# Kernel optimization log

Hardware: AMD Instinct MI355X
Metric: run time of the kernel (lower is better)

## Reference

```python
import jax, jax.numpy as jnp
import numpy as np

B, K, S = 4096, 32, 6          # batch, n_neighbors, n_shifts
QD, H, NH = 512, 384, 6        # query_dim, hidden_dim, n_heads
HD = H // NH                   # head_dim
NR = 20                        # n_residue_types (table has NR+1 rows)
NBR_IN = S + S + 16 + 1 + 1    # neighbor_proj input dim = 30

def gelu(x):
    return jax.nn.gelu(x, approximate=False)

def setup_inputs():
    key = jax.random.key(0)
    ks = iter(jax.random.split(key, 64))
    def nrm(shape, scale=0.05):
        return jax.random.normal(next(ks), shape, dtype=jnp.float32) * scale
    inp = {}
    inp['query_encoding'] = jax.random.normal(next(ks), (B, QD), dtype=jnp.float32)
    inp['query_residue_code'] = jax.random.randint(next(ks), (B,), 0, NR + 1).astype(jnp.int32)
    inp['query_observed_shifts'] = jax.random.normal(next(ks), (B, S), dtype=jnp.float32)
    inp['query_shift_masks'] = (jax.random.uniform(next(ks), (B, S)) < 0.8).astype(jnp.float32)
    inp['retrieved_shifts'] = jax.random.normal(next(ks), (B, K, S), dtype=jnp.float32)
    inp['retrieved_shift_masks'] = jax.random.uniform(next(ks), (B, K, S)) < 0.8
    inp['retrieved_residue_codes'] = jax.random.randint(next(ks), (B, K), 0, NR + 1).astype(jnp.int32)
    inp['retrieved_distances'] = jax.random.uniform(next(ks), (B, K), dtype=jnp.float32)
    inp['retrieved_valid'] = jax.random.uniform(next(ks), (B, K)) < 0.9
    # parameters (buffers + weights). rc_table kept finite (no NaN rows sampled).
    inp['rc_table'] = nrm((NR + 1, S), 1.0)
    inp['W_qp'] = nrm((QD, H)); inp['b_qp'] = jnp.zeros((H,))
    inp['E_res'] = nrm((NR + 1, 16))
    inp['W_np'] = nrm((NBR_IN, H)); inp['b_np'] = jnp.zeros((H,))
    inp['W_aq'] = nrm((H, H)); inp['b_aq'] = jnp.zeros((H,))
    inp['W_ak'] = nrm((H, H)); inp['b_ak'] = jnp.zeros((H,))
    inp['W_av'] = nrm((H, H)); inp['b_av'] = jnp.zeros((H,))
    inp['W_ss1'] = nrm((2 * S, H // 2)); inp['b_ss1'] = jnp.zeros((H // 2,))
    inp['W_ss2'] = nrm((H // 2, NH)); inp['b_ss2'] = jnp.zeros((NH,))
    inp['W_cp1'] = nrm((H, H)); inp['b_cp1'] = jnp.zeros((H,))
    inp['W_cp2'] = nrm((H, H)); inp['b_cp2'] = jnp.zeros((H,))
    inp['W_sw1'] = nrm((H, H)); inp['b_sw1'] = jnp.zeros((H,))
    inp['W_sw2'] = nrm((H, S)); inp['b_sw2'] = jnp.zeros((S,))
    inp['E_trust'] = nrm((NR + 1, 32))
    inp['W_tq'] = nrm((QD, H)); inp['b_tq'] = jnp.zeros((H,))
    inp['W_tc'] = nrm((H + 32 + 4, H)); inp['b_tc'] = jnp.zeros((H,))
    inp['W_tp1'] = nrm((H + 4, H // 2)); inp['b_tp1'] = jnp.zeros((H // 2,))
    inp['W_tp2'] = nrm((H // 2, 1)); inp['b_tp2'] = jnp.zeros((1,))
    inp['shift_scale'] = jnp.ones((S,)); inp['fallback_shift'] = jnp.zeros((S,))
    inp['fallback_context'] = jnp.zeros((H,))
    return inp

def _forward(p):
    eps = 1e-8
    qcode = p['query_residue_code']; rcodes = p['retrieved_residue_codes']
    smask = p['retrieved_shift_masks']; valid = p['retrieved_valid']
    dist = p['retrieved_distances']; rc = p['rc_table']
    # --- RC correction: corrected = RC[query] + (shift - RC[retrieved]) ---
    qidx = jnp.clip(qcode, 0, rc.shape[0] - 1)
    ridx = jnp.clip(rcodes, 0, rc.shape[0] - 1)
    rc_q = rc[qidx][:, None, :]            # (B,1,S)
    rc_r = rc[ridx]                         # (B,K,S)
    corrected = rc_q + (p['retrieved_shifts'] - rc_r)
    rc_valid = (~jnp.isnan(rc_q)) & (~jnp.isnan(rc_r))
    corrected = jnp.where(rc_valid, corrected, p['retrieved_shifts'])
    shifts = jnp.where(smask, corrected, p['retrieved_shifts'])  # (B,K,S)
    any_valid = valid.any(axis=1)                                # (B,)
    same_type = (rcodes == qcode[:, None]).astype(jnp.float32)   # (B,K)
    # --- projections ---
    q = gelu(p['query_encoding'] @ p['W_qp'] + p['b_qp'])        # (B,H)
    res_emb = p['E_res'][rcodes]                                 # (B,K,16)
    nbr = jnp.concatenate([shifts, smask.astype(jnp.float32), res_emb,
                           dist[..., None], same_type[..., None]], axis=-1)
    kv = gelu(nbr @ p['W_np'] + p['b_np'])                       # (B,K,H)
    # --- multi-head cross attention (single query token) ---
    Qh = (q @ p['W_aq'] + p['b_aq']).reshape(B, NH, HD)
    Kh = (kv @ p['W_ak'] + p['b_ak']).reshape(B, K, NH, HD)
    Vh = (kv @ p['W_av'] + p['b_av']).reshape(B, K, NH, HD)
    scores = jnp.einsum('bhd,bkhd->bhk', Qh, Kh) * (HD ** -0.5)  # (B,NH,K)
    sdiff = jnp.concatenate([
        (p['query_observed_shifts'][:, None, :] - shifts) * p['query_shift_masks'][:, None, :],
        jnp.broadcast_to(p['query_shift_masks'][:, None, :], (B, K, S))], axis=-1)
    bias = gelu(sdiff @ p['W_ss1'] + p['b_ss1']) @ p['W_ss2'] + p['b_ss2']  # (B,K,NH)
    scores = scores + jnp.transpose(bias, (0, 2, 1))
    # if nothing valid, unmask slot 0 (matches torch all_masked fixup)
    valid_eff = valid | ((~any_valid)[:, None] & (jnp.arange(K) == 0)[None, :])
    scores = jnp.where(valid_eff[:, None, :], scores, -10000.0)
    w = jax.nn.softmax(scores, axis=-1)
    attn_out = jnp.einsum('bhk,bkhd->bhd', w, Vh).reshape(B, H)
    ctx = gelu(attn_out @ p['W_cp1'] + p['b_cp1']) @ p['W_cp2'] + p['b_cp2']
    ctx = jnp.where(any_valid[:, None], ctx, p['fallback_context'][None, :])
    # --- shift transfer ---
    swb = gelu(attn_out @ p['W_sw1'] + p['b_sw1']) @ p['W_sw2'] + p['b_sw2']  # (B,S)
    weights = dist[..., None] + same_type[..., None] * 0.5 + swb[:, None, :] * 0.1  # (B,K,S)
    valid_mask = valid[..., None] & smask
    weights = jnp.where(valid_mask, weights, -10000.0)
    weights = jax.nn.softmax(weights, axis=1)
    transferred = jnp.sum(weights * shifts, axis=1) * p['shift_scale']
    transferred = jnp.where(any_valid[:, None], transferred, p['fallback_shift'][None, :])
    # --- trust statistics (no grad in original) ---
    vm = valid_mask.astype(jnp.float32)
    cnt = vm.sum(axis=1)                                         # (B,S)
    cov = cnt / (K + eps)
    mean = (shifts * vm).sum(axis=1) / (cnt + eps)
    var = (((shifts - mean[:, None, :]) ** 2) * vm).sum(axis=1) / (cnt + eps)
    var_n = jnp.clip(jnp.log1p(var), 0.0, 5.0) / 5.0
    mdist = (dist[..., None] * vm).sum(axis=1) / (cnt + eps)
    stp = (same_type[..., None] * vm).sum(axis=1) / (cnt + eps)
    per_stats = jax.lax.stop_gradient(jnp.stack([cov, var_n, mdist, stp], axis=-1))  # (B,S,4)
    vf = valid.astype(jnp.float32)
    n_valid = vf.sum(axis=1, keepdims=True) / K
    n_same = (same_type * vf).sum(axis=1, keepdims=True) / K
    dmask = jnp.where(valid, dist, 0.0)
    gmean = dmask.sum(axis=1, keepdims=True) / (vf.sum(axis=1, keepdims=True) + eps)
    gmax = dmask.max(axis=1, keepdims=True)
    gstats = jax.lax.stop_gradient(jnp.concatenate([gmean, gmax, n_valid, n_same], axis=-1))  # (B,4)
    # --- trust head ---
    qre = p['E_trust'][qcode]                                    # (B,32)
    tq = gelu(p['query_encoding'] @ p['W_tq'] + p['b_tq'])
    tc = gelu(jnp.concatenate([tq, qre, gstats], axis=-1) @ p['W_tc'] + p['b_tc'])  # (B,H)
    tin = jnp.concatenate([jnp.broadcast_to(tc[:, None, :], (B, S, H)), per_stats], axis=-1)
    trust = jax.nn.sigmoid(gelu(tin @ p['W_tp1'] + p['b_tp1']) @ p['W_tp2'] + p['b_tp2'])[..., 0]
    return ctx, transferred, trust

def reference(query_encoding, query_residue_code, query_observed_shifts, query_shift_masks,
              retrieved_shifts, retrieved_shift_masks, retrieved_residue_codes,
              retrieved_distances, retrieved_valid, rc_table,
              W_qp, b_qp, E_res, W_np, b_np, W_aq, b_aq, W_ak, b_ak, W_av, b_av,
              W_ss1, b_ss1, W_ss2, b_ss2, W_cp1, b_cp1, W_cp2, b_cp2,
              W_sw1, b_sw1, W_sw2, b_sw2, E_trust, W_tq, b_tq, W_tc, b_tc,
              W_tp1, b_tp1, W_tp2, b_tp2, shift_scale, fallback_shift, fallback_context):
    return _forward(dict(locals()))
```

## Files before the change

### kernel.cpp

```cpp
#include <hip/hip_runtime.h>

typedef unsigned short u16;
typedef unsigned int u32;
typedef __attribute__((ext_vector_type(8))) short bf16x8;
typedef __attribute__((ext_vector_type(4))) float f32x4;

__device__ __forceinline__ float fs(float f) {
    return (f == f && fabsf(f) < 1e30f) ? f : 0.f;
}
__device__ __forceinline__ float fin(float v) {
    return (v == v && fabsf(v) < 1e30f) ? v : 555.0f;
}
__device__ __forceinline__ u16 f2b(float f) {
    union { float f; unsigned int i; } w; w.f = f;
    unsigned int r = w.i + 0x7FFFu + ((w.i >> 16) & 1u);
    return (u16)(r >> 16);
}
__device__ __forceinline__ float b2f(u16 b) {
    union { unsigned int i; float f; } w; w.i = ((unsigned int)b) << 16;
    return w.f;
}
__device__ __forceinline__ float gelu_f(float x) {
    return 0.5f * x * (1.0f + erff(x * 0.70710678118654752440f));
}

__global__ void fill_kernel(float* __restrict__ out, int n, float val) {
    int i = blockIdx.x * 256 + threadIdx.x;
    if (i < n) out[i] = val;
}

struct CvtSrcs { const float* p[13]; };

__global__ void k_cvt_all(CvtSrcs sp, u16* __restrict__ w) {
    int id = blockIdx.x * 256 + threadIdx.x;
    if (id >= 3634304) return;
    if (id < 2097152) { w[id] = f2b(fs(sp.p[0][id])); return; }
    if (id >= 2637824 && id < 2785280) { w[id] = f2b(fs(sp.p[4][id - 2637824])); return; }
    const float* src; int local, K, N, Kp;
    if (id < 2293760)      { src = sp.p[1];  local = id - 2097152; K = 512; N = 384; Kp = 512; }
    else if (id < 2490368) { src = sp.p[2];  local = id - 2293760; K = 512; N = 384; Kp = 512; }
    else if (id < 2637824) { src = sp.p[3];  local = id - 2490368; K = 384; N = 384; Kp = 384; }
    else if (id < 2932736) { src = sp.p[5];  local = id - 2785280; K = 384; N = 384; Kp = 384; }
    else if (id < 3080192) { src = sp.p[6];  local = id - 2932736; K = 384; N = 384; Kp = 384; }
    else if (id < 3227648) { src = sp.p[7];  local = id - 3080192; K = 384; N = 384; Kp = 384; }
    else if (id < 3375104) { src = sp.p[8];  local = id - 3227648; K = 384; N = 384; Kp = 384; }
    else if (id < 3547136) { src = sp.p[9];  local = id - 3375104; K = 420; N = 384; Kp = 448; }
    else if (id < 3620864) { src = sp.p[10]; local = id - 3547136; K = 384; N = 192; Kp = 384; }
    else if (id < 3633152) { src = sp.p[11]; local = id - 3620864; K = 30;  N = 384; Kp = 32;  }
    else                   { src = sp.p[12]; local = id - 3633152; K = 192; N = 6;   Kp = 192; }
    int n = local / Kp, k = local - n * Kp;
    w[id] = (k < K) ? f2b(fs(src[(size_t)k * N + n])) : (u16)0;
}

__global__ void k_prep(const float* __restrict__ qobs, const float* __restrict__ qmask,
                       const float* __restrict__ rshift, const int* __restrict__ rsmask,
                       const int* __restrict__ qcode, const int* __restrict__ rcodes,
                       const float* __restrict__ rdist, const float* __restrict__ rc_table,
                       const float* __restrict__ E_res,
                       float* __restrict__ nbr, float* __restrict__ sdiff, int NBc)
{
    int gk = blockIdx.x * 256 + threadIdx.x;
    if (gk >= NBc) return;
    int b = gk >> 5;
    int qc = qcode[b], rc = rcodes[gk];
    int qi = min(max(qc, 0), 20), ri = min(max(rc, 0), 20);
    float dist = fs(rdist[gk]);
    float same = (rc == qc) ? 1.f : 0.f;
    float* nr = nbr + (size_t)gk * 30;
    float* sd = sdiff + (size_t)gk * 12;
    for (int s = 0; s < 6; s++) {
        float rs = fs(rshift[gk * 6 + s]);
        bool m = rsmask[gk * 6 + s] != 0;
        float rq = rc_table[qi * 6 + s];
        float rr = rc_table[ri * 6 + s];
        bool rcv = (rq == rq) && (rr == rr) && fabsf(rq) < 1e30f && fabsf(rr) < 1e30f;
        float sh = (m && rcv) ? (rq + rs - rr) : rs;
        nr[s] = sh;
        nr[6 + s] = m ? 1.f : 0.f;
        float qm = fs(qmask[b * 6 + s]);
        sd[s] = (fs(qobs[b * 6 + s]) - sh) * qm;
        sd[6 + s] = qm;
    }
    for (int j = 0; j < 16; j++) nr[12 + j] = fs(E_res[ri * 16 + j]);
    nr[28] = dist;
    nr[29] = same;
}

__global__ void k_stats_w(const float* __restrict__ nbr, const int* __restrict__ rvalid,
                          float* __restrict__ pst, float* __restrict__ gst,
                          float* __restrict__ anyv, int BCc)
{
    int wid = (blockIdx.x * 256 + threadIdx.x) >> 6;
    int lane = threadIdx.x & 63;
    if (wid >= BCc * 4) return;
    int b = wid >> 2, sub = wid & 3;
    if (sub < 3) {
        int s = sub * 2 + (lane >> 5), k = lane & 31;
        const float* nr = nbr + (size_t)(b * 32 + k) * 30;
        float vf = (rvalid[b * 32 + k] != 0) ? 1.f : 0.f;
        float vm = vf * nr[6 + s];
        float shv = nr[s], dist = nr[28], same = nr[29];
        float cnt = vm, msum = shv * vm, mdist = dist * vm, mst = same * vm;
#pragma unroll
        for (int m = 1; m <= 16; m <<= 1) {
            cnt += __shfl_xor(cnt, m);
            msum += __shfl_xor(msum, m);
            mdist += __shfl_xor(mdist, m);
            mst += __shfl_xor(mst, m);
        }
        float inv = 1.f / (cnt + 1e-8f);
        float mean = msum * inv;
        float dv = shv - mean;
        float var = dv * dv * vm;
#pragma unroll
        for (int m = 1; m <= 16; m <<= 1) var += __shfl_xor(var, m);
        var *= inv;
        if (k == 0) {
            float* p = pst + (size_t)b * 24 + s * 4;
            p[0] = cnt * (1.f / 32.f);
            p[1] = fminf(fmaxf(log1pf(var), 0.f), 5.f) * 0.2f;
            p[2] = mdist * inv;
            p[3] = mst * inv;
        }
    } else {
        int k = lane & 31;
        float svf = 0.f, sdm = 0.f, mdm = -1e30f, ssm = 0.f;
        if (lane < 32) {
            const float* nr = nbr + (size_t)(b * 32 + k) * 30;
            float vf = (rvalid[b * 32 + k] != 0) ? 1.f : 0.f;
            float dm = vf * nr[28];
            svf = vf; sdm = dm; mdm = dm; ssm = vf * nr[29];
        }
#pragma unroll
        for (int m = 1; m <= 32; m <<= 1) {
            svf += __shfl_xor(svf, m);
            sdm += __shfl_xor(sdm, m);
            mdm = fmaxf(mdm, __shfl_xor(mdm, m));
            ssm += __shfl_xor(ssm, m);
        }
        if (lane == 0) {
            float* g = gst + (size_t)b * 4;
            g[0] = sdm / (svf + 1e-8f);
            g[1] = mdm;
            g[2] = svf * (1.f / 32.f);
            g[3] = ssm * (1.f / 32.f);
            anyv[b] = (svf > 0.f) ? 1.f : 0.f;
        }
    }
}

template <int ACT, bool OUTF, bool OUTB>
__device__ __forceinline__ void gemm_body(
    const u16* __restrict__ A, int lda,
    const u16* __restrict__ BT, int ldb,
    const float* __restrict__ bias, const float* __restrict__ bias1,
    float* __restrict__ Cf, u16* __restrict__ Cb, int ldc,
    int K, int m0, int n0)
{
    __shared__ u16 As[64 * 72];
    __shared__ u16 Bs[64 * 72];
    const int t = threadIdx.x;
    const int lane = t & 63, wave = t >> 6;
    const int wm = (wave & 1) << 5, wn = (wave >> 1) << 5;
    const int frm = lane & 15, frq = lane >> 4;
    const int r0 = t >> 3, c0 = (t & 7) << 3;
    const f32x4 z = {0.f, 0.f, 0.f, 0.f};
    f32x4 acc[2][2] = {{z, z}, {z, z}};
    for (int k0 = 0; k0 < K; k0 += 64) {
        *(bf16x8*)&As[r0 * 72 + c0]        = *(const bf16x8*)&A[(size_t)(m0 + r0) * lda + k0 + c0];
        *(bf16x8*)&As[(r0 + 32) * 72 + c0] = *(const bf16x8*)&A[(size_t)(m0 + r0 + 32) * lda + k0 + c0];
        *(bf16x8*)&Bs[r0 * 72 + c0]        = *(const bf16x8*)&BT[(size_t)(n0 + r0) * ldb + k0 + c0];
        *(bf16x8*)&Bs[(r0 + 32) * 72 + c0] = *(const bf16x8*)&BT[(size_t)(n0 + r0 + 32) * ldb + k0 + c0];
        __syncthreads();
#pragma unroll
        for (int kk = 0; kk < 2; kk++) {
            const int fo = (kk << 5) + (frq << 3);
            bf16x8 a0 = *(const bf16x8*)&As[(wm + frm) * 72 + fo];
            bf16x8 a1 = *(const bf16x8*)&As[(wm + 16 + frm) * 72 + fo];
            bf16x8 b0 = *(const bf16x8*)&Bs[(wn + frm) * 72 + fo];
            bf16x8 b1 = *(const bf16x8*)&Bs[(wn + 16 + frm) * 72 + fo];
            acc[0][0] = __builtin_amdgcn_mfma_f32_16x16x32_bf16(a0, b0, acc[0][0], 0, 0, 0);
            acc[0][1] = __builtin_amdgcn_mfma_f32_16x16x32_bf16(a0, b1, acc[0][1], 0, 0, 0);
            acc[1][0] = __builtin_amdgcn_mfma_f32_16x16x32_bf16(a1, b0, acc[1][0], 0, 0, 0);
            acc[1][1] = __builtin_amdgcn_mfma_f32_16x16x32_bf16(a1, b1, acc[1][1], 0, 0, 0);
        }
        __syncthreads();
    }
#pragma unroll
    for (int mi = 0; mi < 2; mi++) {
#pragma unroll
        for (int ni = 0; ni < 2; ni++) {
            int col = n0 + wn + (ni << 4) + frm;
            float bv = 0.f;
            if (bias) {
                if (bias1 && col >= 384) bv = fs(bias1[col - 384]);
                else bv = fs(bias[col]);
            }
#pragma unroll
            for (int r = 0; r < 4; r++) {
                int row = m0 + wm + (mi << 4) + (frq << 2) + r;
                float v = acc[mi][ni][r] + bv;
                if (ACT == 1) v = gelu_f(v);
                if (OUTF) Cf[(size_t)row * ldc + col] = v;
                if (OUTB) Cb[(size_t)row * ldc + col] = f2b(v);
            }
        }
    }
}

template <int ACT, bool OUTF, bool OUTB>
__global__ __launch_bounds__(256) void k_gemm_bb(
    const u16* __restrict__ A, int lda, const u16* __restrict__ BT, int ldb,
    const float* __restrict__ bias, float* __restrict__ Cf, u16* __restrict__ Cb,
    int ldc, int K)
{
    gemm_body<ACT, OUTF, OUTB>(A, lda, BT, ldb, bias, nullptr, Cf, Cb, ldc, K,
                               blockIdx.y << 6, blockIdx.x << 6);
}

template <int ACT>
__global__ __launch_bounds__(256) void k_gemm_bb2(
    const u16* __restrict__ A, int lda, const u16* __restrict__ BT, int ldb,
    const float* __restrict__ bias0, const float* __restrict__ bias1,
    u16* __restrict__ Cb, int ldc, int K)
{
    gemm_body<ACT, false, true>(A, lda, BT, ldb, bias0, bias1, nullptr, Cb, ldc, K,
                                blockIdx.y << 6, blockIdx.x << 6);
}

__global__ __launch_bounds__(256) void k_gemm_ctx(
    const u16* __restrict__ A, int lda, const u16* __restrict__ BT, int ldb,
    const float* __restrict__ bias, const float* __restrict__ anyv,
    const float* __restrict__ fctx, float* __restrict__ outp, int ldc, int K)
{
    __shared__ u16 As[64 * 72];
    __shared__ u16 Bs[64 * 72];
    const int t = threadIdx.x;
    const int lane = t & 63, wave = t >> 6;
    const int m0 = blockIdx.y << 6, n0 = blockIdx.x << 6;
    const int wm = (wave & 1) << 5, wn = (wave >> 1) << 5;
    const int frm = lane & 15, frq = lane >> 4;
    const int r0 = t >> 3, c0 = (t & 7) << 3;
    const f32x4 z = {0.f, 0.f, 0.f, 0.f};
    f32x4 acc[2][2] = {{z, z}, {z, z}};
    for (int k0 = 0; k0 < K; k0 += 64) {
        *(bf16x8*)&As[r0 * 72 + c0]        = *(const bf16x8*)&A[(size_t)(m0 + r0) * lda + k0 + c0];
        *(bf16x8*)&As[(r0 + 32) * 72 + c0] = *(const bf16x8*)&A[(size_t)(m0 + r0 + 32) * lda + k0 + c0];
        *(bf16x8*)&Bs[r0 * 72 + c0]        = *(const bf16x8*)&BT[(size_t)(n0 + r0) * ldb + k0 + c0];
        *(bf16x8*)&Bs[(r0 + 32) * 72 + c0] = *(const bf16x8*)&BT[(size_t)(n0 + r0 + 32) * ldb + k0 + c0];
        __syncthreads();
#pragma unroll
        for (int kk = 0; kk < 2; kk++) {
            const int fo = (kk << 5) + (frq << 3);
            bf16x8 a0 = *(const bf16x8*)&As[(wm + frm) * 72 + fo];
            bf16x8 a1 = *(const bf16x8*)&As[(wm + 16 + frm) * 72 + fo];
            bf16x8 b0 = *(const bf16x8*)&Bs[(wn + frm) * 72 + fo];
            bf16x8 b1 = *(const bf16x8*)&Bs[(wn + 16 + frm) * 72 + fo];
            acc[0][0] = __builtin_amdgcn_mfma_f32_16x16x32_bf16(a0, b0, acc[0][0], 0, 0, 0);
            acc[0][1] = __builtin_amdgcn_mfma_f32_16x16x32_bf16(a0, b1, acc[0][1], 0, 0, 0);
            acc[1][0] = __builtin_amdgcn_mfma_f32_16x16x32_bf16(a1, b0, acc[1][0], 0, 0, 0);
            acc[1][1] = __builtin_amdgcn_mfma_f32_16x16x32_bf16(a1, b1, acc[1][1], 0, 0, 0);
        }
        __syncthreads();
    }
#pragma unroll
    for (int mi = 0; mi < 2; mi++) {
#pragma unroll
        for (int ni = 0; ni < 2; ni++) {
            int col = n0 + wn + (ni << 4) + frm;
            float bv = fs(bias[col]);
            float fv = fs(fctx[col]);
#pragma unroll
            for (int r = 0; r < 4; r++) {
                int row = m0 + wm + (mi << 4) + (frq << 2) + r;
                float v = acc[mi][ni][r] + bv;
                v = (anyv[row] > 0.f) ? v : fv;
                outp[(size_t)row * ldc + col] = fin(v);
            }
        }
    }
}

__global__ __launch_bounds__(256) void k_qp_loop(
    const u16* __restrict__ Qhb, const u16* __restrict__ WakB, u16* __restrict__ Qpb)
{
    __shared__ u16 As[64 * 72];
    __shared__ u16 Bs[64 * 72];
    const int t = threadIdx.x;
    const int lane = t & 63, wave = t >> 6;
    const int m0 = blockIdx.x << 6, hd = blockIdx.y;
    const int wm = (wave & 1) << 5, wn = (wave >> 1) << 5;
    const int frm = lane & 15, frq = lane >> 4;
    const int r0 = t >> 3, c0 = (t & 7) << 3;
    const f32x4 z = {0.f, 0.f, 0.f, 0.f};
    *(bf16x8*)&As[r0 * 72 + c0]        = *(const bf16x8*)&Qhb[(size_t)(m0 + r0) * 384 + hd * 64 + c0];
    *(bf16x8*)&As[(r0 + 32) * 72 + c0] = *(const bf16x8*)&Qhb[(size_t)(m0 + r0 + 32) * 384 + hd * 64 + c0];
    for (int nt = 0; nt < 6; nt++) {
        *(bf16x8*)&Bs[r0 * 72 + c0]        = *(const bf16x8*)&WakB[(size_t)(nt * 64 + r0) * 384 + hd * 64 + c0];
        *(bf16x8*)&Bs[(r0 + 32) * 72 + c0] = *(const bf16x8*)&WakB[(size_t)(nt * 64 + r0 + 32) * 384 + hd * 64 + c0];
        __syncthreads();
        f32x4 acc[2][2] = {{z, z}, {z, z}};
#pragma unroll
        for (int kk = 0; kk < 2; kk++) {
            const int fo = (kk << 5) + (frq << 3);
            bf16x8 a0 = *(const bf16x8*)&As[(wm + frm) * 72 + fo];
            bf16x8 a1 = *(const bf16x8*)&As[(wm + 16 + frm) * 72 + fo];
            bf16x8 b0 = *(const bf16x8*)&Bs[(wn + frm) * 72 + fo];
            bf16x8 b1 = *(const bf16x8*)&Bs[(wn + 16 + frm) * 72 + fo];
            acc[0][0] = __builtin_amdgcn_mfma_f32_16x16x32_bf16(a0, b0, acc[0][0], 0, 0, 0);
            acc[0][1] = __builtin_amdgcn_mfma_f32_16x16x32_bf16(a0, b1, acc[0][1], 0, 0, 0);
            acc[1][0] = __builtin_amdgcn_mfma_f32_16x16x32_bf16(a1, b0, acc[1][0], 0, 0, 0);
            acc[1][1] = __builtin_amdgcn_mfma_f32_16x16x32_bf16(a1, b1, acc[1][1], 0, 0, 0);
        }
#pragma unroll
        for (int mi = 0; mi < 2; mi++) {
#pragma unroll
            for (int ni = 0; ni < 2; ni++) {
                int col = nt * 64 + wn + (ni << 4) + frm;
#pragma unroll
                for (int r = 0; r < 4; r++) {
                    int row = m0 + wm + (mi << 4) + (frq << 2) + r;
                    Qpb[(size_t)row * 2304 + hd * 384 + col] = f2b(acc[mi][ni][r]);
                }
            }
        }
        __syncthreads();
    }
}

__global__ __launch_bounds__(256) void k_attnout_bb(
    const u16* __restrict__ vmsb, const u16* __restrict__ WavT,
    const float* __restrict__ bav, u16* __restrict__ attnb)
{
    int hd = blockIdx.x;
    gemm_body<0, false, true>(vmsb + hd * 384, 2304, WavT + (size_t)hd * 64 * 384, 384,
                              bav + hd * 64, nullptr, nullptr, attnb + hd * 64, 384, 384,
                              blockIdx.y << 6, 0);
}

__global__ __launch_bounds__(192) void k_mlpbias(
    const float* __restrict__ sdiff, const float* __restrict__ Wss1,
    const float* __restrict__ bss1, const u16* __restrict__ Wss2T,
    const float* __restrict__ bss2, float* __restrict__ bias_s)
{
    __shared__ float sdS[32 * 12];
    __shared__ u16 hidSb[32 * 200];
    const int b = blockIdx.x;
    const int t = threadIdx.x;
    for (int i = t; i < 384; i += 192) sdS[i] = sdiff[(size_t)b * 384 + i];
    __syncthreads();
    {
        float w[12];
#pragma unroll
        for (int j = 0; j < 12; j++) w[j] = fs(Wss1[j * 192 + t]);
        float b1 = fs(bss1[t]);
        for (int k = 0; k < 32; k++) {
            float acc = b1;
#pragma unroll
            for (int j = 0; j < 12; j++) acc += sdS[k * 12 + j] * w[j];
            hidSb[k * 200 + t] = f2b(gelu_f(acc));
        }
    }
    __syncthreads();
    if (t < 64) {
        const int frm = t & 15, frq = t >> 4;
        const f32x4 z = {0.f, 0.f, 0.f, 0.f};
        f32x4 acc0 = z, acc1 = z;
        const u16* bt = Wss2T + (frm < 6 ? frm : 0) * 192;
#pragma unroll
        for (int ks = 0; ks < 6; ks++) {
            bf16x8 bf = *(const bf16x8*)&bt[ks * 32 + (frq << 3)];
            bf16x8 a0 = *(const bf16x8*)&hidSb[frm * 200 + ks * 32 + (frq << 3)];
            bf16x8 a1 = *(const bf16x8*)&hidSb[(16 + frm) * 200 + ks * 32 + (frq << 3)];
            acc0 = __builtin_amdgcn_mfma_f32_16x16x32_bf16(a0, bf, acc0, 0, 0, 0);
            acc1 = __builtin_amdgcn_mfma_f32_16x16x32_bf16(a1, bf, acc1, 0, 0, 0);
        }
        if (frm < 6) {
            float bb = fs(bss2[frm]);
#pragma unroll
            for (int r = 0; r < 4; r++) {
                int kk = (frq << 2) + r;
                bias_s[(size_t)(b * 32 + kk) * 6 + frm] = acc0[r] + bb;
                bias_s[(size_t)(b * 32 + kk + 16) * 6 + frm] = acc1[r] + bb;
            }
        }
    }
}

__global__ void k_qkb_w(const u16* __restrict__ Qhb, const float* __restrict__ bak,
                        float* __restrict__ qkb, int BCc)
{
    int wid = (blockIdx.x * 256 + threadIdx.x) >> 6;
    int lane = threadIdx.x & 63;
    if (wid >= BCc * 6) return;
    int b = wid / 6, h = wid - b * 6;
    float acc = b2f(Qhb[(size_t)b * 384 + h * 64 + lane]) * fs(bak[h * 64 + lane]);
#pragma unroll
    for (int m = 1; m <= 32; m <<= 1) acc += __shfl_xor(acc, m);
    if (lane == 0) qkb[b * 6 + h] = acc;
}

__global__ __launch_bounds__(384) void k_attnblk(
    const float* __restrict__ nbr, const u16* __restrict__ WnpT,
    const float* __restrict__ bnp, const u16* __restrict__ Qpb,
    const float* __restrict__ qkb, const float* __restrict__ bias_s,
    const int* __restrict__ rvalid, const float* __restrict__ anyv,
    u16* __restrict__ vmsb)
{
    __shared__ u16 kvsb[32 * 392];
    __shared__ u16 qSb[6 * 392];
    __shared__ float wsx[192];
    __shared__ float uSf[512];
    u16* aS = (u16*)uSf;
    float* sS = uSf;
    const int b = blockIdx.x;
    const int t = threadIdx.x;
    const int lane = t & 63, wave = t >> 6;
    const int frm = lane & 15, frq = lane >> 4;
    for (int i = t; i < 1152; i += 384) {
        int h = i / 192, k2 = i - h * 192;
        ((u32*)qSb)[h * 196 + k2] = ((const u32*)(Qpb + (size_t)b * 2304))[i];
    }
    {
        const float* nr = nbr + (size_t)b * 960;
        for (int i = t; i < 1024; i += 384) {
            int r = i >> 5, cc = i & 31;
            aS[r * 32 + cc] = (cc < 30) ? f2b(nr[r * 30 + cc]) : (u16)0;
        }
    }
    __syncthreads();
    {
        bf16x8 a0 = *(const bf16x8*)&aS[frm * 32 + (frq << 3)];
        bf16x8 a1 = *(const bf16x8*)&aS[(16 + frm) * 32 + (frq << 3)];
        const f32x4 z = {0.f, 0.f, 0.f, 0.f};
        f32x4 acc0[4] = {z, z, z, z};
        f32x4 acc1[4] = {z, z, z, z};
#pragma unroll
        for (int ct = 0; ct < 4; ct++) {
            int col = (wave << 6) + (ct << 4) + frm;
            bf16x8 bf = *(const bf16x8*)&WnpT[col * 32 + (frq << 3)];
            acc0[ct] = __builtin_amdgcn_mfma_f32_16x16x32_bf16(a0, bf, acc0[ct], 0, 0, 0);
            acc1[ct] = __builtin_amdgcn_mfma_f32_16x16x32_bf16(a1, bf, acc1[ct], 0, 0, 0);
        }
#pragma unroll
        for (int ct = 0; ct < 4; ct++) {
            int col = (wave << 6) + (ct << 4) + frm;
            float bb = fs(bnp[col]);
#pragma unroll
            for (int r = 0; r < 4; r++) {
                int row0 = (frq << 2) + r;
                kvsb[row0 * 392 + col] = f2b(gelu_f(acc0[ct][r] + bb));
                kvsb[(row0 + 16) * 392 + col] = f2b(gelu_f(acc1[ct][r] + bb));
            }
        }
    }
    __syncthreads();
    if (wave < 2) {
        f32x4 accs = {0.f, 0.f, 0.f, 0.f};
#pragma unroll
        for (int ks = 0; ks < 12; ks++) {
            bf16x8 af = *(const bf16x8*)&kvsb[((wave << 4) + frm) * 392 + (ks << 5) + (frq << 3)];
            int hh = (frm < 6) ? frm : 0;
            bf16x8 bf = *(const bf16x8*)&qSb[hh * 392 + (ks << 5) + (frq << 3)];
            accs = __builtin_amdgcn_mfma_f32_16x16x32_bf16(af, bf, accs, 0, 0, 0);
        }
        if (frm < 6) {
#pragma unroll
            for (int r = 0; r < 4; r++)
                sS[((wave << 4) + (frq << 2) + r) * 8 + frm] = accs[r];
        }
    }
    __syncthreads();
    if (t < 192) {
        int h = t >> 5, k = t & 31;
        float s = (sS[k * 8 + h] + qkb[b * 6 + h]) * 0.125f
                + bias_s[(size_t)(b * 32 + k) * 6 + h];
        bool ve = (rvalid[b * 32 + k] != 0) || (anyv[b] == 0.f && k == 0);
        s = ve ? s : -10000.f;
        float mx = s;
        mx = fmaxf(mx, __shfl_xor(mx, 1));
        mx = fmaxf(mx, __shfl_xor(mx, 2));
        mx = fmaxf(mx, __shfl_xor(mx, 4));
        mx = fmaxf(mx, __shfl_xor(mx, 8));
        mx = fmaxf(mx, __shfl_xor(mx, 16));
        float e = expf(s - mx);
        float sum = e;
        sum += __shfl_xor(sum, 1);
        sum += __shfl_xor(sum, 2);
        sum += __shfl_xor(sum, 4);
        sum += __shfl_xor(sum, 8);
        sum += __shfl_xor(sum, 16);
        wsx[h * 32 + k] = e / sum;
    }
    __syncthreads();
    {
        float a0 = 0.f, a1 = 0.f, a2 = 0.f, a3 = 0.f, a4 = 0.f, a5 = 0.f;
        for (int k = 0; k < 32; k++) {
            float kvv = b2f(kvsb[k * 392 + t]);
            a0 += wsx[k] * kvv;
            a1 += wsx[32 + k] * kvv;
            a2 += wsx[64 + k] * kvv;
            a3 += wsx[96 + k] * kvv;
            a4 += wsx[128 + k] * kvv;
            a5 += wsx[160 + k] * kvv;
        }
        u16* vp = vmsb + (size_t)b * 2304;
        vp[t] = f2b(a0);
        vp[384 + t] = f2b(a1);
        vp[768 + t] = f2b(a2);
        vp[1152 + t] = f2b(a3);
        vp[1536 + t] = f2b(a4);
        vp[1920 + t] = f2b(a5);
    }
}

__global__ void k_xtc_b(const u16* __restrict__ qtqb, const int* __restrict__ qcode,
                        const float* __restrict__ Etr, const float* __restrict__ gst,
                        u16* __restrict__ Xb, int BCc)
{
    int id = blockIdx.x * 256 + threadIdx.x;
    if (id >= BCc * 448) return;
    int b = id / 448, c = id - b * 448;
    if (c < 384) { Xb[id] = qtqb[(size_t)b * 768 + 384 + c]; return; }
    float v;
    if (c < 416) v = fs(Etr[min(max(qcode[b], 0), 20) * 32 + (c - 384)]);
    else if (c < 420) v = gst[(size_t)b * 4 + (c - 416)];
    else v = 0.f;
    Xb[id] = f2b(v);
}

__global__ void k_swb_w(const u16* __restrict__ hs1b, const float* __restrict__ Wsw2,
                        const float* __restrict__ bsw2, float* __restrict__ swb, int BCc)
{
    int wid = (blockIdx.x * 256 + threadIdx.x) >> 6;
    int lane = threadIdx.x & 63;
    if (wid >= BCc * 6) return;
    int b = wid / 6, s = wid - b * 6;
    float acc = 0.f;
#pragma unroll
    for (int i = 0; i < 6; i++) {
        int n = lane + 64 * i;
        acc += b2f(hs1b[(size_t)b * 768 + 384 + n]) * fs(Wsw2[n * 6 + s]);
    }
#pragma unroll
    for (int m = 1; m <= 32; m <<= 1) acc += __shfl_xor(acc, m);
    if (lane == 0) swb[b * 6 + s] = acc + fs(bsw2[s]);
}

__global__ void k_tail_w(const float* __restrict__ tcp, const float* __restrict__ pst,
                         const float* __restrict__ Wtp1, const float* __restrict__ Wtp2,
                         const float* __restrict__ btp2, float* __restrict__ outT,
                         const float* __restrict__ nbr, const int* __restrict__ rsmask,
                         const int* __restrict__ rvalid, const float* __restrict__ swb,
                         const float* __restrict__ anyv, const float* __restrict__ sscale,
                         const float* __restrict__ fshift, float* __restrict__ outX, int BCc)
{
    int wid = (blockIdx.x * 256 + threadIdx.x) >> 6;
    int lane = threadIdx.x & 63;
    if (wid >= BCc * 9) return;
    int b = wid / 9, sub = wid - b * 9;
    if (sub < 6) {
        int s = sub;
        const float* ps = pst + (size_t)b * 24 + s * 4;
        float p0 = ps[0], p1 = ps[1], p2 = ps[2], p3 = ps[3];
        float acc = 0.f;
#pragma unroll
        for (int i = 0; i < 3; i++) {
            int j = lane + 64 * i;
            float pre = tcp[(size_t)b * 192 + j];
            pre += p0 * fs(Wtp1[(size_t)384 * 192 + j]);
            pre += p1 * fs(Wtp1[(size_t)385 * 192 + j]);
            pre += p2 * fs(Wtp1[(size_t)386 * 192 + j]);
            pre += p3 * fs(Wtp1[(size_t)387 * 192 + j]);
            acc += gelu_f(pre) * fs(Wtp2[j]);
        }
#pragma unroll
        for (int m = 1; m <= 32; m <<= 1) acc += __shfl_xor(acc, m);
        if (lane == 0) {
            float tv = 1.f / (1.f + expf(-(acc + fs(btp2[0]))));
            outT[b * 6 + s] = fin(tv);
        }
    } else {
        int s2 = sub - 6;
        int s = s2 * 2 + (lane >> 5), k = lane & 31;
        if (anyv[b] <= 0.f) {
            if (k == 0) outX[b * 6 + s] = fin(fs(fshift[s]));
            return;
        }
        int gk = b * 32 + k;
        const float* nr = nbr + (size_t)gk * 30;
        float wb = swb[b * 6 + s] * 0.1f;
        bool m = (rvalid[gk] != 0) && (rsmask[gk * 6 + s] != 0);
        float wv = m ? (nr[28] + nr[29] * 0.5f + wb) : -10000.f;
        float mx = wv;
#pragma unroll
        for (int mm = 1; mm <= 16; mm <<= 1) mx = fmaxf(mx, __shfl_xor(mx, mm));
        float e = expf(wv - mx);
        float num = e * nr[s], den = e;
#pragma unroll
        for (int mm = 1; mm <= 16; mm <<= 1) {
            num += __shfl_xor(num, mm);
            den += __shfl_xor(den, mm);
        }
        if (k == 0) outX[b * 6 + s] = fin((num / den) * fs(sscale[s]));
    }
}

#define L1(total) <<<((total) + 255) / 256, 256, 0, stream>>>
#define LW(nwaves) <<<(((nwaves) * 64) + 255) / 256, 256, 0, stream>>>

extern "C" void kernel_launch(void* const* d_in, const int* in_sizes, int n_in,
                              void* d_out, int out_size, void* d_ws, size_t ws_size,
                              hipStream_t stream)
{
    float* out = (float*)d_out;

    static const int EXP[45] = {
        2097152, 4096, 24576, 24576, 786432, 786432, 131072, 131072, 131072, 126,
        196608, 384, 336, 11520, 384, 147456, 384, 147456, 384, 147456, 384,
        2304, 192, 1152, 6, 147456, 384, 147456, 384, 147456, 384, 2304, 6,
        672, 196608, 384, 161280, 384, 74496, 192, 192, 1, 6, 6, 384
    };
    if (n_in != 45) {
        fill_kernel L1(out_size)(out, out_size, 580.0f);
        return;
    }
    for (int i = 0; i < 45; i++) {
        if (in_sizes[i] != EXP[i]) {
            fill_kernel L1(out_size)(out, out_size, 600.0f + 4.0f * i);
            return;
        }
    }

    const float* i_qe    = (const float*)d_in[0];
    const int*   i_qcode = (const int*)d_in[1];
    const float* i_qobs  = (const float*)d_in[2];
    const float* i_qmask = (const float*)d_in[3];
    const float* i_rshift= (const float*)d_in[4];
    const int*   i_rsmask= (const int*)d_in[5];
    const int*   i_rcodes= (const int*)d_in[6];
    const float* i_rdist = (const float*)d_in[7];
    const int*   i_rvalid= (const int*)d_in[8];
    const float* i_rc    = (const float*)d_in[9];
    const float* i_Wqp   = (const float*)d_in[10];
    const float* i_bqp   = (const float*)d_in[11];
    const float* i_Eres  = (const float*)d_in[12];
    const float* i_Wnp   = (const float*)d_in[13];
    const float* i_bnp   = (const float*)d_in[14];
    const float* i_Waq   = (const float*)d_in[15];
    const float* i_baq   = (const float*)d_in[16];
    const float* i_Wak   = (const float*)d_in[17];
    const float* i_bak   = (const float*)d_in[18];
    const float* i_Wav   = (const float*)d_in[19];
    const float* i_bav   = (const float*)d_in[20];
    const float* i_Wss1  = (const float*)d_in[21];
    const float* i_bss1  = (const float*)d_in[22];
    const float* i_Wss2  = (const float*)d_in[23];
    const float* i_bss2  = (const float*)d_in[24];
    const float* i_Wcp1  = (const float*)d_in[25];
    const float* i_bcp1  = (const float*)d_in[26];
    const float* i_Wcp2  = (const float*)d_in[27];
    const float* i_bcp2  = (const float*)d_in[28];
    const float* i_Wsw1  = (const float*)d_in[29];
    const float* i_bsw1  = (const float*)d_in[30];
    const float* i_Wsw2  = (const float*)d_in[31];
    const float* i_bsw2  = (const float*)d_in[32];
    const float* i_Etr   = (const float*)d_in[33];
    const float* i_Wtq   = (const float*)d_in[34];
    const float* i_btq   = (const float*)d_in[35];
    const float* i_Wtc   = (const float*)d_in[36];
    const float* i_btc   = (const float*)d_in[37];
    const float* i_Wtp1  = (const float*)d_in[38];
    const float* i_btp1  = (const float*)d_in[39];
    const float* i_Wtp2  = (const float*)d_in[40];
    const float* i_btp2  = (const float*)d_in[41];
    const float* i_sscale= (const float*)d_in[42];
    const float* i_fshift= (const float*)d_in[43];
    const float* i_fctx  = (const float*)d_in[44];

    auto layoutBytes = [](int bc) -> size_t {
        auto al = [](size_t x) { return (x + 255) & ~(size_t)255; };
        size_t off = 0;
        off += al(3634304ull * 2);
        size_t nb = (size_t)bc * 32;
        off += al(nb * 30 * 4) + al(nb * 12 * 4) + al(nb * 6 * 4);
        off += al((size_t)bc * 192 * 4);
        off += al((size_t)bc * 2304 * 2) * 2;
        off += al((size_t)bc * 768 * 2) * 2;
        off += al((size_t)bc * 384 * 2) * 3;
        off += al((size_t)bc * 448 * 2);
        off += al((size_t)bc * 6 * 4) * 2 + al((size_t)bc * 24 * 4)
             + al((size_t)bc * 4 * 4) + al((size_t)bc * 4);
        return off;
    };
    const int cand[7] = {4096, 2048, 1024, 512, 256, 128, 64};
    int BCc = 64;
    for (int i = 0; i < 7; i++) {
        if (layoutBytes(cand[i]) <= ws_size) { BCc = cand[i]; break; }
    }
    const int NBc = BCc * 32;

    char* wsb = (char*)d_ws;
    size_t off = 0;
    auto allocB = [&](size_t bytes) -> void* {
        void* p = (void*)(wsb + off);
        off = (off + bytes + 255) & ~(size_t)255;
        return p;
    };
    u16* wsW = (u16*)allocB(3634304ull * 2);
    u16* qeb   = wsW;
    u16* WqtqT = wsW + 2097152;
    u16* WaqT  = wsW + 2490368;
    u16* WakB  = wsW + 2637824;
    u16* WavT  = wsW + 2785280;
    u16* Wcp2T = wsW + 2932736;
    u16* Whs1T = wsW + 3080192;
    u16* WtcT  = wsW + 3375104;
    u16* Wtp1T = wsW + 3547136;
    u16* WnpT  = wsW + 3620864;
    u16* Wss2T = wsW + 3633152;
    float* nbr   = (float*)allocB((size_t)NBc * 30 * 4);
    float* sdiff = (float*)allocB((size_t)NBc * 12 * 4);
    float* bias_s= (float*)allocB((size_t)NBc * 6 * 4);
    float* tcpf  = (float*)allocB((size_t)BCc * 192 * 4);
    u16*   Qpb   = (u16*)allocB((size_t)BCc * 2304 * 2);
    u16*   vmsb  = (u16*)allocB((size_t)BCc * 2304 * 2);
    u16*   qtqb  = (u16*)allocB((size_t)BCc * 768 * 2);
    u16*   hs1b  = (u16*)allocB((size_t)BCc * 768 * 2);
    u16*   Qhb   = (u16*)allocB((size_t)BCc * 384 * 2);
    u16*   attnb = (u16*)allocB((size_t)BCc * 384 * 2);
    u16*   tcb   = (u16*)allocB((size_t)BCc * 384 * 2);
    u16*   Xfb   = (u16*)allocB((size_t)BCc * 448 * 2);
    float* swbf  = (float*)allocB((size_t)BCc * 6 * 4);
    float* qkbf  = (float*)allocB((size_t)BCc * 6 * 4);
    float* pstf  = (float*)allocB((size_t)BCc * 24 * 4);
    float* gstf  = (float*)allocB((size_t)BCc * 4 * 4);
    float* anyf  = (float*)allocB((size_t)BCc * 4);

    if (off > ws_size) {
        fill_kernel L1(out_size)(out, out_size, 1000.0f);
        return;
    }

    CvtSrcs sp;
    sp.p[0] = i_qe;  sp.p[1] = i_Wqp;  sp.p[2] = i_Wtq;  sp.p[3] = i_Waq;
    sp.p[4] = i_Wak; sp.p[5] = i_Wav;  sp.p[6] = i_Wcp2; sp.p[7] = i_Wcp1;
    sp.p[8] = i_Wsw1; sp.p[9] = i_Wtc; sp.p[10] = i_Wtp1; sp.p[11] = i_Wnp;
    sp.p[12] = i_Wss2;
    k_cvt_all L1(3634304)(sp, wsW);

    for (int c = 0; c < 4096 / BCc; c++) {
        const size_t B0 = (size_t)c * BCc;
        const dim3 g6(6, BCc / 64), g3(3, BCc / 64), g12(12, BCc / 64);
        const dim3 gqp(BCc / 64, 6), gao(6, BCc / 64);
        k_prep L1(NBc)(i_qobs + B0 * 6, i_qmask + B0 * 6, i_rshift + B0 * 192,
                       i_rsmask + B0 * 192, i_qcode + B0, i_rcodes + B0 * 32,
                       i_rdist + B0 * 32, i_rc, i_Eres, nbr, sdiff, NBc);
        k_stats_w LW(BCc * 4)(nbr, i_rvalid + B0 * 32, pstf, gstf, anyf, BCc);
        k_mlpbias<<<BCc, 192, 0, stream>>>(sdiff, i_Wss1, i_bss1, Wss2T, i_bss2, bias_s);
        k_gemm_bb2<1><<<g12, 256, 0, stream>>>(
            qeb + B0 * 512, 512, WqtqT, 512, i_bqp, i_btq, qtqb, 768, 512);
        k_gemm_bb<0, false, true><<<g6, 256, 0, stream>>>(
            qtqb, 768, WaqT, 384, i_baq, nullptr, Qhb, 384, 384);
        k_qp_loop<<<gqp, 256, 0, stream>>>(Qhb, WakB, Qpb);
        k_qkb_w LW(BCc * 6)(Qhb, i_bak, qkbf, BCc);
        k_attnblk<<<BCc, 384, 0, stream>>>(nbr, WnpT, i_bnp, Qpb, qkbf, bias_s,
                                           i_rvalid + B0 * 32, anyf, vmsb);
        k_attnout_bb<<<gao, 256, 0, stream>>>(vmsb, WavT, i_bav, attnb);
        k_gemm_bb2<1><<<g12, 256, 0, stream>>>(
            attnb, 384, Whs1T, 384, i_bcp1, i_bsw1, hs1b, 768, 384);
        k_gemm_ctx<<<g6, 256, 0, stream>>>(
            hs1b, 768, Wcp2T, 384, i_bcp2, anyf, i_fctx, out + B0 * 384, 384, 384);
        k_swb_w LW(BCc * 6)(hs1b, i_Wsw2, i_bsw2, swbf, BCc);
        k_xtc_b L1(BCc * 448)(qtqb, i_qcode + B0, i_Etr, gstf, Xfb, BCc);
        k_gemm_bb<1, false, true><<<g6, 256, 0, stream>>>(
            Xfb, 448, WtcT, 448, i_btc, nullptr, tcb, 384, 448);
        k_gemm_bb<0, true, false><<<g3, 256, 0, stream>>>(
            tcb, 384, Wtp1T, 384, i_btp1, tcpf, nullptr, 192, 384);
        k_tail_w LW(BCc * 9)(tcpf, pstf, i_Wtp1, i_Wtp2, i_btp2,
                             out + (size_t)4096 * 390 + B0 * 6,
                             nbr, i_rsmask + B0 * 192, i_rvalid + B0 * 32, swbf, anyf,
                             i_sscale, i_fshift, out + (size_t)4096 * 384 + B0 * 6, BCc);
    }
}
```

Baseline: 393.5 us.

## Use 128-row GEMM tiles, fuse concat into trust GEMM and qk-bias into qp

Result: no change. 396.8 us (median of 2 runs) (+0.8%).

```diff
diff --git a/kernel.cpp b/kernel.cpp
--- a/kernel.cpp
+++ b/kernel.cpp
@@ -150,44 +150,48 @@
 }
 
 template <int ACT, bool OUTF, bool OUTB>
-__device__ __forceinline__ void gemm_body(
+__device__ __forceinline__ void gemm_body128(
     const u16* __restrict__ A, int lda,
     const u16* __restrict__ BT, int ldb,
     const float* __restrict__ bias, const float* __restrict__ bias1,
     float* __restrict__ Cf, u16* __restrict__ Cb, int ldc,
     int K, int m0, int n0)
 {
-    __shared__ u16 As[64 * 72];
+    __shared__ u16 As[128 * 72];
     __shared__ u16 Bs[64 * 72];
     const int t = threadIdx.x;
     const int lane = t & 63, wave = t >> 6;
-    const int wm = (wave & 1) << 5, wn = (wave >> 1) << 5;
+    const int wm = (wave & 1) << 6, wn = (wave >> 1) << 5;
     const int frm = lane & 15, frq = lane >> 4;
     const int r0 = t >> 3, c0 = (t & 7) << 3;
     const f32x4 z = {0.f, 0.f, 0.f, 0.f};
-    f32x4 acc[2][2] = {{z, z}, {z, z}};
+    f32x4 acc[4][2] = {{z, z}, {z, z}, {z, z}, {z, z}};
     for (int k0 = 0; k0 < K; k0 += 64) {
-        *(bf16x8*)&As[r0 * 72 + c0]        = *(const bf16x8*)&A[(size_t)(m0 + r0) * lda + k0 + c0];
-        *(bf16x8*)&As[(r0 + 32) * 72 + c0] = *(const bf16x8*)&A[(size_t)(m0 + r0 + 32) * lda + k0 + c0];
-        *(bf16x8*)&Bs[r0 * 72 + c0]        = *(const bf16x8*)&BT[(size_t)(n0 + r0) * ldb + k0 + c0];
-        *(bf16x8*)&Bs[(r0 + 32) * 72 + c0] = *(const bf16x8*)&BT[(size_t)(n0 + r0 + 32) * ldb + k0 + c0];
+#pragma unroll
+        for (int i = 0; i < 4; i++)
+            *(bf16x8*)&As[(r0 + 32 * i) * 72 + c0] =
+                *(const bf16x8*)&A[(size_t)(m0 + r0 + 32 * i) * lda + k0 + c0];
+#pragma unroll
+        for (int i = 0; i < 2; i++)
+            *(bf16x8*)&Bs[(r0 + 32 * i) * 72 + c0] =
+                *(const bf16x8*)&BT[(size_t)(n0 + r0 + 32 * i) * ldb + k0 + c0];
         __syncthreads();
 #pragma unroll
         for (int kk = 0; kk < 2; kk++) {
             const int fo = (kk << 5) + (frq << 3);
-            bf16x8 a0 = *(const bf16x8*)&As[(wm + frm) * 72 + fo];
-            bf16x8 a1 = *(const bf16x8*)&As[(wm + 16 + frm) * 72 + fo];
             bf16x8 b0 = *(const bf16x8*)&Bs[(wn + frm) * 72 + fo];
             bf16x8 b1 = *(const bf16x8*)&Bs[(wn + 16 + frm) * 72 + fo];
-            acc[0][0] = __builtin_amdgcn_mfma_f32_16x16x32_bf16(a0, b0, acc[0][0], 0, 0, 0);
-            acc[0][1] = __builtin_amdgcn_mfma_f32_16x16x32_bf16(a0, b1, acc[0][1], 0, 0, 0);
-            acc[1][0] = __builtin_amdgcn_mfma_f32_16x16x32_bf16(a1, b0, acc[1][0], 0, 0, 0);
-            acc[1][1] = __builtin_amdgcn_mfma_f32_16x16x32_bf16(a1, b1, acc[1][1], 0, 0, 0);
+#pragma unroll
+            for (int mi = 0; mi < 4; mi++) {
+                bf16x8 a = *(const bf16x8*)&As[(wm + (mi << 4) + frm) * 72 + fo];
+                acc[mi][0] = __builtin_amdgcn_mfma_f32_16x16x32_bf16(a, b0, acc[mi][0], 0, 0, 0);
+                acc[mi][1] = __builtin_amdgcn_mfma_f32_16x16x32_bf16(a, b1, acc[mi][1], 0, 0, 0);
+            }
         }
         __syncthreads();
     }
 #pragma unroll
-    for (int mi = 0; mi < 2; mi++) {
+    for (int mi = 0; mi < 4; mi++) {
 #pragma unroll
         for (int ni = 0; ni < 2; ni++) {
             int col = n0 + wn + (ni << 4) + frm;
@@ -214,8 +218,8 @@
     const float* __restrict__ bias, float* __restrict__ Cf, u16* __restrict__ Cb,
     int ldc, int K)
 {
-    gemm_body<ACT, OUTF, OUTB>(A, lda, BT, ldb, bias, nullptr, Cf, Cb, ldc, K,
-                               blockIdx.y << 6, blockIdx.x << 6);
+    gemm_body128<ACT, OUTF, OUTB>(A, lda, BT, ldb, bias, nullptr, Cf, Cb, ldc, K,
+                                  blockIdx.y << 7, blockIdx.x << 6);
 }
 
 template <int ACT>
@@ -224,8 +228,8 @@
     const float* __restrict__ bias0, const float* __restrict__ bias1,
     u16* __restrict__ Cb, int ldc, int K)
 {
-    gemm_body<ACT, false, true>(A, lda, BT, ldb, bias0, bias1, nullptr, Cb, ldc, K,
-                                blockIdx.y << 6, blockIdx.x << 6);
+    gemm_body128<ACT, false, true>(A, lda, BT, ldb, bias0, bias1, nullptr, Cb, ldc, K,
+                                   blockIdx.y << 7, blockIdx.x << 6);
 }
 
 __global__ __launch_bounds__(256) void k_gemm_ctx(
@@ -233,38 +237,42 @@
     const float* __restrict__ bias, const float* __restrict__ anyv,
     const float* __restrict__ fctx, float* __restrict__ outp, int ldc, int K)
 {
-    __shared__ u16 As[64 * 72];
+    __shared__ u16 As[128 * 72];
     __shared__ u16 Bs[64 * 72];
     const int t = threadIdx.x;
     const int lane = t & 63, wave = t >> 6;
-    const int m0 = blockIdx.y << 6, n0 = blockIdx.x << 6;
-    const int wm = (wave & 1) << 5, wn = (wave >> 1) << 5;
+    const int m0 = blockIdx.y << 7, n0 = blockIdx.x << 6;
+    const int wm = (wave & 1) << 6, wn = (wave >> 1) << 5;
     const int frm = lane & 15, frq = lane >> 4;
     const int r0 = t >> 3, c0 = (t & 7) << 3;
     const f32x4 z = {0.f, 0.f, 0.f, 0.f};
-    f32x4 acc[2][2] = {{z, z}, {z, z}};
+    f32x4 acc[4][2] = {{z, z}, {z, z}, {z, z}, {z, z}};
     for (int k0 = 0; k0 < K; k0 += 64) {
-        *(bf16x8*)&As[r0 * 72 + c0]        = *(const bf16x8*)&A[(size_t)(m0 + r0) * lda + k0 + c0];
-        *(bf16x8*)&As[(r0 + 32) * 72 + c0] = *(const bf16x8*)&A[(size_t)(m0 + r0 + 32) * lda + k0 + c0];
-        *(bf16x8*)&Bs[r0 * 72 + c0]        = *(const bf16x8*)&BT[(size_t)(n0 + r0) * ldb + k0 + c0];
-        *(bf16x8*)&Bs[(r0 + 32) * 72 + c0] = *(const bf16x8*)&BT[(size_t)(n0 + r0 + 32) * ldb + k0 + c0];
+#pragma unroll
+        for (int i = 0; i < 4; i++)
+            *(bf16x8*)&As[(r0 + 32 * i) * 72 + c0] =
+                *(const bf16x8*)&A[(size_t)(m0 + r0 + 32 * i) * lda + k0 + c0];
+#pragma unroll
+        for (int i = 0; i < 2; i++)
+            *(bf16x8*)&Bs[(r0 + 32 * i) * 72 + c0] =
+                *(const bf16x8*)&BT[(size_t)(n0 + r0 + 32 * i) * ldb + k0 + c0];
         __syncthreads();
 #pragma unroll
         for (int kk = 0; kk < 2; kk++) {
             const int fo = (kk << 5) + (frq << 3);
-            bf16x8 a0 = *(const bf16x8*)&As[(wm + frm) * 72 + fo];
-            bf16x8 a1 = *(const bf16x8*)&As[(wm + 16 + frm) * 72 + fo];
             bf16x8 b0 = *(const bf16x8*)&Bs[(wn + frm) * 72 + fo];
             bf16x8 b1 = *(const bf16x8*)&Bs[(wn + 16 + frm) * 72 + fo];
-            acc[0][0] = __builtin_amdgcn_mfma_f32_16x16x32_bf16(a0, b0, acc[0][0], 0, 0, 0);
-            acc[0][1] = __builtin_amdgcn_mfma_f32_16x16x32_bf16(a0, b1, acc[0][1], 0, 0, 0);
-            acc[1][0] = __builtin_amdgcn_mfma_f32_16x16x32_bf16(a1, b0, acc[1][0], 0, 0, 0);
-            acc[1][1] = __builtin_amdgcn_mfma_f32_16x16x32_bf16(a1, b1, acc[1][1], 0, 0, 0);
+#pragma unroll
+            for (int mi = 0; mi < 4; mi++) {
+                bf16x8 a = *(const bf16x8*)&As[(wm + (mi << 4) + frm) * 72 + fo];
+                acc[mi][0] = __builtin_amdgcn_mfma_f32_16x16x32_bf16(a, b0, acc[mi][0], 0, 0, 0);
+                acc[mi][1] = __builtin_amdgcn_mfma_f32_16x16x32_bf16(a, b1, acc[mi][1], 0, 0, 0);
+            }
         }
         __syncthreads();
     }
 #pragma unroll
-    for (int mi = 0; mi < 2; mi++) {
+    for (int mi = 0; mi < 4; mi++) {
 #pragma unroll
         for (int ni = 0; ni < 2; ni++) {
             int col = n0 + wn + (ni << 4) + frm;
@@ -281,8 +289,81 @@
     }
 }
 
+__global__ __launch_bounds__(256) void k_gemm_tc(
+    const u16* __restrict__ qtqb, const int* __restrict__ qcode,
+    const float* __restrict__ Etr, const float* __restrict__ gst,
+    const u16* __restrict__ BT, const float* __restrict__ bias,
+    u16* __restrict__ Cb)
+{
+    __shared__ u16 As[128 * 72];
+    __shared__ u16 Bs[64 * 72];
+    const int t = threadIdx.x;
+    const int lane = t & 63, wave = t >> 6;
+    const int m0 = blockIdx.y << 7, n0 = blockIdx.x << 6;
+    const int wm = (wave & 1) << 6, wn = (wave >> 1) << 5;
+    const int frm = lane & 15, frq = lane >> 4;
+    const int r0 = t >> 3, c0 = (t & 7) << 3;
+    const f32x4 z = {0.f, 0.f, 0.f, 0.f};
+    f32x4 acc[4][2] = {{z, z}, {z, z}, {z, z}, {z, z}};
+    for (int k0 = 0; k0 < 448; k0 += 64) {
+        if (k0 < 384) {
+#pragma unroll
+            for (int i = 0; i < 4; i++)
+                *(bf16x8*)&As[(r0 + 32 * i) * 72 + c0] =
+                    *(const bf16x8*)&qtqb[(size_t)(m0 + r0 + 32 * i) * 768 + 384 + k0 + c0];
+        } else {
+#pragma unroll
+            for (int i = 0; i < 4; i++) {
+                int row = m0 + r0 + 32 * i;
+                int qi = min(max(qcode[row], 0), 20);
+#pragma unroll
+                for (int j = 0; j < 8; j++) {
+                    int col = k0 + c0 + j;
+                    u16 v;
+                    if (col < 416) v = f2b(fs(Etr[qi * 32 + (col - 384)]));
+                    else if (col < 420) v = f2b(gst[(size_t)row * 4 + (col - 416)]);
+                    else v = (u16)0;
+                    As[(r0 + 32 * i) * 72 + c0 + j] = v;
+                }
+            }
+        }
+#pragma unroll
+        for (int i = 0; i < 2; i++)
+            *(bf16x8*)&Bs[(r0 + 32 * i) * 72 + c0] =
+                *(const bf16x8*)&BT[(size_t)(n0 + r0 + 32 * i) * 448 + k0 + c0];
+        __syncthreads();
+#pragma unroll
+        for (int kk = 0; kk < 2; kk++) {
+            const int fo = (kk << 5) + (frq << 3);
+            bf16x8 b0 = *(const bf16x8*)&Bs[(wn + frm) * 72 + fo];
+            bf16x8 b1 = *(const bf16x8*)&Bs[(wn + 16 + frm) * 72 + fo];
+#pragma unroll
+            for (int mi = 0; mi < 4; mi++) {
+                bf16x8 a = *(const bf16x8*)&As[(wm + (mi << 4) + frm) * 72 + fo];
+                acc[mi][0] = __builtin_amdgcn_mfma_f32_16x16x32_bf16(a, b0, acc[mi][0], 0, 0, 0);
+                acc[mi][1] = __builtin_amdgcn_mfma_f32_16x16x32_bf16(a, b1, acc[mi][1], 0, 0, 0);
+            }
+        }
+        __syncthreads();
+    }
+#pragma unroll
+    for (int mi = 0; mi < 4; mi++) {
+#pragma unroll
+        for (int ni = 0; ni < 2; ni++) {
+            int col = n0 + wn + (ni << 4) + frm;
+            float bv = fs(bias[col]);
+#pragma unroll
+            for (int r = 0; r < 4; r++) {
+                int row = m0 + wm + (mi << 4) + (frq << 2) + r;
+                Cb[(size_t)row * 384 + col] = f2b(gelu_f(acc[mi][ni][r] + bv));
+            }
+        }
+    }
+}
+
 __global__ __launch_bounds__(256) void k_qp_loop(
-    const u16* __restrict__ Qhb, const u16* __restrict__ WakB, u16* __restrict__ Qpb)
+    const u16* __restrict__ Qhb, const u16* __restrict__ WakB,
+    const float* __restrict__ bak, u16* __restrict__ Qpb, float* __restrict__ qkb)
 {
     __shared__ u16 As[64 * 72];
     __shared__ u16 Bs[64 * 72];
@@ -295,6 +376,19 @@
     const f32x4 z = {0.f, 0.f, 0.f, 0.f};
     *(bf16x8*)&As[r0 * 72 + c0]        = *(const bf16x8*)&Qhb[(size_t)(m0 + r0) * 384 + hd * 64 + c0];
     *(bf16x8*)&As[(r0 + 32) * 72 + c0] = *(const bf16x8*)&Qhb[(size_t)(m0 + r0 + 32) * 384 + hd * 64 + c0];
+    __syncthreads();
+    {
+        int r = t >> 2, p = t & 3;
+        float acc = 0.f;
+#pragma unroll
+        for (int i = 0; i < 16; i++) {
+            int d = p * 16 + i;
+            acc += b2f(As[r * 72 + d]) * fs(bak[hd * 64 + d]);
+        }
+        acc += __shfl_xor(acc, 1);
+        acc += __shfl_xor(acc, 2);
+        if (p == 0) qkb[(m0 + r) * 6 + hd] = acc;
+    }
     for (int nt = 0; nt < 6; nt++) {
         *(bf16x8*)&Bs[r0 * 72 + c0]        = *(const bf16x8*)&WakB[(size_t)(nt * 64 + r0) * 384 + hd * 64 + c0];
         *(bf16x8*)&Bs[(r0 + 32) * 72 + c0] = *(const bf16x8*)&WakB[(size_t)(nt * 64 + r0 + 32) * 384 + hd * 64 + c0];
@@ -333,9 +427,9 @@
     const float* __restrict__ bav, u16* __restrict__ attnb)
 {
     int hd = blockIdx.x;
-    gemm_body<0, false, true>(vmsb + hd * 384, 2304, WavT + (size_t)hd * 64 * 384, 384,
-                              bav + hd * 64, nullptr, nullptr, attnb + hd * 64, 384, 384,
-                              blockIdx.y << 6, 0);
+    gemm_body128<0, false, true>(vmsb + hd * 384, 2304, WavT + (size_t)hd * 64 * 384, 384,
+                                 bav + hd * 64, nullptr, nullptr, attnb + hd * 64, 384, 384,
+                                 blockIdx.y << 7, 0);
 }
 
 __global__ __launch_bounds__(192) void k_mlpbias(
@@ -385,19 +479,6 @@
             }
         }
     }
-}
-
-__global__ void k_qkb_w(const u16* __restrict__ Qhb, const float* __restrict__ bak,
-                        float* __restrict__ qkb, int BCc)
-{
-    int wid = (blockIdx.x * 256 + threadIdx.x) >> 6;
-    int lane = threadIdx.x & 63;
-    if (wid >= BCc * 6) return;
-    int b = wid / 6, h = wid - b * 6;
-    float acc = b2f(Qhb[(size_t)b * 384 + h * 64 + lane]) * fs(bak[h * 64 + lane]);
-#pragma unroll
-    for (int m = 1; m <= 32; m <<= 1) acc += __shfl_xor(acc, m);
-    if (lane == 0) qkb[b * 6 + h] = acc;
 }
 
 __global__ __launch_bounds__(384) void k_attnblk(
@@ -512,21 +593,6 @@
         vp[1536 + t] = f2b(a4);
         vp[1920 + t] = f2b(a5);
     }
-}
-
-__global__ void k_xtc_b(const u16* __restrict__ qtqb, const int* __restrict__ qcode,
-                        const float* __restrict__ Etr, const float* __restrict__ gst,
-                        u16* __restrict__ Xb, int BCc)
-{
-    int id = blockIdx.x * 256 + threadIdx.x;
-    if (id >= BCc * 448) return;
-    int b = id / 448, c = id - b * 448;
-    if (c < 384) { Xb[id] = qtqb[(size_t)b * 768 + 384 + c]; return; }
-    float v;
-    if (c < 416) v = fs(Etr[min(max(qcode[b], 0), 20) * 32 + (c - 384)]);
-    else if (c < 420) v = gst[(size_t)b * 4 + (c - 416)];
-    else v = 0.f;
-    Xb[id] = f2b(v);
 }
 
 __global__ void k_swb_w(const u16* __restrict__ hs1b, const float* __restrict__ Wsw2,
@@ -688,14 +754,13 @@
         off += al((size_t)bc * 2304 * 2) * 2;
         off += al((size_t)bc * 768 * 2) * 2;
         off += al((size_t)bc * 384 * 2) * 3;
-        off += al((size_t)bc * 448 * 2);
         off += al((size_t)bc * 6 * 4) * 2 + al((size_t)bc * 24 * 4)
              + al((size_t)bc * 4 * 4) + al((size_t)bc * 4);
         return off;
     };
-    const int cand[7] = {4096, 2048, 1024, 512, 256, 128, 64};
-    int BCc = 64;
-    for (int i = 0; i < 7; i++) {
+    const int cand[6] = {4096, 2048, 1024, 512, 256, 128};
+    int BCc = 128;
+    for (int i = 0; i < 6; i++) {
         if (layoutBytes(cand[i]) <= ws_size) { BCc = cand[i]; break; }
     }
     const int NBc = BCc * 32;
@@ -730,7 +795,6 @@
     u16*   Qhb   = (u16*)allocB((size_t)BCc * 384 * 2);
     u16*   attnb = (u16*)allocB((size_t)BCc * 384 * 2);
     u16*   tcb   = (u16*)allocB((size_t)BCc * 384 * 2);
-    u16*   Xfb   = (u16*)allocB((size_t)BCc * 448 * 2);
     float* swbf  = (float*)allocB((size_t)BCc * 6 * 4);
     float* qkbf  = (float*)allocB((size_t)BCc * 6 * 4);
     float* pstf  = (float*)allocB((size_t)BCc * 24 * 4);
@@ -751,8 +815,9 @@
 
     for (int c = 0; c < 4096 / BCc; c++) {
         const size_t B0 = (size_t)c * BCc;
-        const dim3 g6(6, BCc / 64), g3(3, BCc / 64), g12(12, BCc / 64);
-        const dim3 gqp(BCc / 64, 6), gao(6, BCc / 64);
+        const int MB = BCc / 128;
+        const dim3 g6(6, MB), g3(3, MB), g12(12, MB), gao(6, MB);
+        const dim3 gqp(BCc / 64, 6);
         k_prep L1(NBc)(i_qobs + B0 * 6, i_qmask + B0 * 6, i_rshift + B0 * 192,
                        i_rsmask + B0 * 192, i_qcode + B0, i_rcodes + B0 * 32,
                        i_rdist + B0 * 32, i_rc, i_Eres, nbr, sdiff, NBc);
@@ -762,8 +827,7 @@
             qeb + B0 * 512, 512, WqtqT, 512, i_bqp, i_btq, qtqb, 768, 512);
         k_gemm_bb<0, false, true><<<g6, 256, 0, stream>>>(
             qtqb, 768, WaqT, 384, i_baq, nullptr, Qhb, 384, 384);
-        k_qp_loop<<<gqp, 256, 0, stream>>>(Qhb, WakB, Qpb);
-        k_qkb_w LW(BCc * 6)(Qhb, i_bak, qkbf, BCc);
+        k_qp_loop<<<gqp, 256, 0, stream>>>(Qhb, WakB, i_bak, Qpb, qkbf);
         k_attnblk<<<BCc, 384, 0, stream>>>(nbr, WnpT, i_bnp, Qpb, qkbf, bias_s,
                                            i_rvalid + B0 * 32, anyf, vmsb);
         k_attnout_bb<<<gao, 256, 0, stream>>>(vmsb, WavT, i_bav, attnb);
@@ -772,9 +836,8 @@
         k_gemm_ctx<<<g6, 256, 0, stream>>>(
             hs1b, 768, Wcp2T, 384, i_bcp2, anyf, i_fctx, out + B0 * 384, 384, 384);
         k_swb_w LW(BCc * 6)(hs1b, i_Wsw2, i_bsw2, swbf, BCc);
-        k_xtc_b L1(BCc * 448)(qtqb, i_qcode + B0, i_Etr, gstf, Xfb, BCc);
-        k_gemm_bb<1, false, true><<<g6, 256, 0, stream>>>(
-            Xfb, 448, WtcT, 448, i_btc, nullptr, tcb, 384, 448);
+        k_gemm_tc<<<g6, 256, 0, stream>>>(
+            qtqb, i_qcode + B0, i_Etr, gstf, WtcT, i_btc, tcb);
         k_gemm_bb<0, true, false><<<g3, 256, 0, stream>>>(
             tcb, 384, Wtp1T, 384, i_btp1, tcpf, nullptr, 192, 384);
         k_tail_w LW(BCc * 9)(tcpf, pstf, i_Wtp1, i_Wtp2, i_btp2,
```
